# Kernel tuning notes

Hardware: AMD Instinct MI355X
Metric: run time of the kernel (lower is better)

## Reference

```python
import jax, jax.numpy as jnp
import numpy as np


def setup_inputs() -> dict:
    key = jax.random.key(0)
    k1, k2 = jax.random.split(key)
    in_features, out_features = 4096, 4096
    tokens = 8192
    x = jax.random.normal(k1, (tokens, in_features), dtype=jnp.float32)
    # matches reset_parameters: N(0, sqrt(1/in_features))
    weight = jax.random.normal(k2, (out_features, in_features), dtype=jnp.float32) * np.sqrt(1.0 / in_features)
    bias = jnp.zeros((out_features,), dtype=jnp.float32)
    return {"x": x, "weight": weight, "bias": bias}


def reference(x, weight, bias):
    # BinaryLinearFunction.forward: binarize weight to sign(w), dense matmul, add bias
    w_bin = jnp.sign(weight)  # [out, in], values in {-1, 0, +1}
    return x @ w_bin.T + bias  # [tokens, out]
```

## Files before the change

### kernel.cpp

```cpp
#include <hip/hip_runtime.h>
#include <stdint.h>
#include <stddef.h>

typedef int i32x4 __attribute__((ext_vector_type(4)));

static constexpr int M = 8192, N = 4096, K = 4096;
static constexpr int BM = 128, BN = 128, BK = 128;


__global__ __launch_bounds__(256) void quant_rows(const float* __restrict__ x,
                                                  int8_t* __restrict__ xq,
                                                  float* __restrict__ scales) {
    const int row = blockIdx.x;
    const int tid = threadIdx.x;
    const float4* xr = (const float4*)(x + (size_t)row * K);

    float4 v[4];
    float m = 0.f;
#pragma unroll
    for (int k = 0; k < 4; ++k) {
        v[k] = xr[k * 256 + tid];
        m = fmaxf(m, fmaxf(fmaxf(fabsf(v[k].x), fabsf(v[k].y)),
                           fmaxf(fabsf(v[k].z), fabsf(v[k].w))));
    }
#pragma unroll
    for (int off = 32; off; off >>= 1) m = fmaxf(m, __shfl_down(m, off, 64));

    __shared__ float wm[4];
    if ((tid & 63) == 0) wm[tid >> 6] = m;
    __syncthreads();
    const float amax = fmaxf(fmaxf(fmaxf(wm[0], wm[1]), fmaxf(wm[2], wm[3])), 1e-20f);
    const float s = 127.0f / amax;
    if (tid == 0) scales[row] = amax * (1.0f / 127.0f);

    int8_t* xo = xq + (size_t)row * K;
#pragma unroll
    for (int k = 0; k < 4; ++k) {
        int8_t o[4] = {(int8_t)__float2int_rn(v[k].x * s),
                       (int8_t)__float2int_rn(v[k].y * s),
                       (int8_t)__float2int_rn(v[k].z * s),
                       (int8_t)__float2int_rn(v[k].w * s)};
        *(int*)(xo + (k * 256 + tid) * 4) = *(const int*)o;
    }
}

__global__ __launch_bounds__(256) void binarize_w_kernel(const float* __restrict__ w,
                                                         int8_t* __restrict__ wq) {
    const size_t i = (size_t)blockIdx.x * 256 + threadIdx.x;
    float4 a = ((const float4*)w)[i];
    float vv[4] = {a.x, a.y, a.z, a.w};
    int8_t o[4];
#pragma unroll
    for (int j = 0; j < 4; ++j)
        o[j] = (vv[j] > 0.f) ? (int8_t)1 : ((vv[j] < 0.f) ? (int8_t)-1 : (int8_t)0);
    *(int*)(wq + 4 * i) = *(const int*)o;
}


__device__ __forceinline__ void async_copy16(const int8_t* g, int8_t* l) {
    __builtin_amdgcn_global_load_lds(
        (const __attribute__((address_space(1))) void*)g,
        (__attribute__((address_space(3))) void*)l,
        16, 0, 0);
}

__global__ __launch_bounds__(256) void gemm_i8(const int8_t* __restrict__ A,
                                               const int8_t* __restrict__ B,
                                               const float* __restrict__ bias,
                                               const float* __restrict__ scales,
                                               float* __restrict__ C) {
    __shared__ __align__(16) int8_t As[BM * BK];
    __shared__ __align__(16) int8_t Bs[BN * BK];

    const int tid  = threadIdx.x;
    const int lane = tid & 63;
    const int wave = tid >> 6;
    const int m0 = blockIdx.y * BM;
    const int n0 = blockIdx.x * BN;

    const int wr = wave >> 1, wc = wave & 1;
    const int q  = lane >> 4;
    const int lr = lane & 15;

    i32x4 acc[4][4];
#pragma unroll
    for (int i = 0; i < 4; ++i)
#pragma unroll
        for (int j = 0; j < 4; ++j) acc[i][j] = (i32x4)0;

    const int8_t* gA[4];
    const int8_t* gB[4];
#pragma unroll
    for (int j = 0; j < 4; ++j) {
        int s = tid + 256 * j;
        int r = s >> 3, c = s & 7;
        int cs = c ^ (r & 7);
        gA[j] = A + (size_t)(m0 + r) * K + cs * 16;
        gB[j] = B + (size_t)(n0 + r) * K + cs * 16;
    }

    int aoff[4], boff[4];
#pragma unroll
    for (int mi = 0; mi < 4; ++mi) {
        int r  = wr * 64 + mi * 16 + lr;
        aoff[mi] = (r * 8 + (q ^ (r & 7))) * 16;
        int rb = wc * 64 + mi * 16 + lr;
        boff[mi] = (rb * 8 + (q ^ (rb & 7))) * 16;
    }

    for (int kt = 0; kt < K / BK; ++kt) {
        const int kofs = kt * BK;
#pragma unroll
        for (int j = 0; j < 4; ++j) async_copy16(gA[j] + kofs, As + (tid + 256 * j) * 16);
#pragma unroll
        for (int j = 0; j < 4; ++j) async_copy16(gB[j] + kofs, Bs + (tid + 256 * j) * 16);
        __syncthreads();

#pragma unroll
        for (int ks = 0; ks < 2; ++ks) {
            const int kx = ks << 6;
            i32x4 af[4], bfr[4];
#pragma unroll
            for (int mi = 0; mi < 4; ++mi) af[mi]  = *(const i32x4*)(As + (aoff[mi] ^ kx));
#pragma unroll
            for (int ni = 0; ni < 4; ++ni) bfr[ni] = *(const i32x4*)(Bs + (boff[ni] ^ kx));
#pragma unroll
            for (int mi = 0; mi < 4; ++mi)
#pragma unroll
                for (int ni = 0; ni < 4; ++ni)
                    acc[mi][ni] = __builtin_amdgcn_mfma_i32_16x16x64_i8(
                        af[mi], bfr[ni], acc[mi][ni], 0, 0, 0);
        }
        __syncthreads();
    }

    float srow[4][4];
#pragma unroll
    for (int mi = 0; mi < 4; ++mi) {
        int row0 = m0 + wr * 64 + mi * 16 + q * 4;
#pragma unroll
        for (int i = 0; i < 4; ++i) srow[mi][i] = scales[row0 + i];
    }
#pragma unroll
    for (int ni = 0; ni < 4; ++ni) {
        int col = n0 + wc * 64 + ni * 16 + lr;
        float bv = bias[col];
#pragma unroll
        for (int mi = 0; mi < 4; ++mi) {
            int row0 = m0 + wr * 64 + mi * 16 + q * 4;
#pragma unroll
            for (int i = 0; i < 4; ++i)
                C[(size_t)(row0 + i) * N + col] = (float)acc[mi][ni][i] * srow[mi][i] + bv;
        }
    }
}


extern "C" void kernel_launch(void* const* d_in, const int* in_sizes, int n_in,
                              void* d_out, int out_size, void* d_ws, size_t ws_size,
                              hipStream_t stream) {
    const float* x    = (const float*)d_in[0];
    const float* w    = (const float*)d_in[1];
    const float* bias = (const float*)d_in[2];
    float* out        = (float*)d_out;

    float* scales = (float*)d_ws;
    int8_t* xq = (int8_t*)d_ws + 32768;
    int8_t* wq = xq + (size_t)M * K;

    quant_rows<<<M, 256, 0, stream>>>(x, xq, scales);
    binarize_w_kernel<<<(N * K / 4) / 256, 256, 0, stream>>>(w, wq);

    dim3 grid(N / BN, M / BM);
    gemm_i8<<<grid, 256, 0, stream>>>(xq, wq, bias, scales, out);
}
```

Baseline: 414.1 us.

## Double-buffer 256x256 int8 GEMM tiles with async LDS prefetch and block swizzle

Enlarges the GEMM tile to 256x256 with 512 threads, splits each K step into two 64-wide halves held in double-buffered shared memory, and prefetches the next stages with async global-to-LDS copies paced by explicit vmcnt waits. It also swizzles the block order on a 1D grid for L2 reuse and raises wave priority around MFMA bursts. The aim is to overlap memory loads with MFMA work and cut redundant global traffic. In exchange it uses much more LDS per block, which limits occupancy, and depends on hand-written waitcnt correctness.

```diff
diff --git a/kernel.cpp b/kernel.cpp
--- a/kernel.cpp
+++ b/kernel.cpp
@@ -5,7 +5,8 @@
 typedef int i32x4 __attribute__((ext_vector_type(4)));
 
 static constexpr int M = 8192, N = 4096, K = 4096;
-static constexpr int BM = 128, BN = 128, BK = 128;
+static constexpr int BM = 256, BN = 256, BK = 128;
+static constexpr int NT = K / BK;
 
 
 __global__ __launch_bounds__(256) void quant_rows(const float* __restrict__ x,
@@ -64,90 +65,136 @@
         16, 0, 0);
 }
 
-__global__ __launch_bounds__(256) void gemm_i8(const int8_t* __restrict__ A,
-                                               const int8_t* __restrict__ B,
-                                               const float* __restrict__ bias,
-                                               const float* __restrict__ scales,
-                                               float* __restrict__ C) {
-    __shared__ __align__(16) int8_t As[BM * BK];
-    __shared__ __align__(16) int8_t Bs[BN * BK];
+#define FENCE() asm volatile("" ::: "memory")
+#define BAR() do { FENCE(); __builtin_amdgcn_s_barrier(); FENCE(); } while (0)
+#define WAITVM(NN) asm volatile("s_waitcnt vmcnt(" #NN ")" ::: "memory")
+
+__global__ __launch_bounds__(512, 2) void gemm_i8(const int8_t* __restrict__ A,
+                                                  const int8_t* __restrict__ B,
+                                                  const float* __restrict__ bias,
+                                                  const float* __restrict__ scales,
+                                                  float* __restrict__ C) {
+    __shared__ __align__(16) int8_t As[2][2][BM * 64];
+    __shared__ __align__(16) int8_t Bs[2][2][BN * 64];
 
     const int tid  = threadIdx.x;
     const int lane = tid & 63;
     const int wave = tid >> 6;
-    const int m0 = blockIdx.y * BM;
-    const int n0 = blockIdx.x * BN;
-
-    const int wr = wave >> 1, wc = wave & 1;
+    const int wr = wave >> 2;
+    const int wc = wave & 3;
     const int q  = lane >> 4;
     const int lr = lane & 15;
 
-    i32x4 acc[4][4];
-#pragma unroll
-    for (int i = 0; i < 4; ++i)
-#pragma unroll
-        for (int j = 0; j < 4; ++j) acc[i][j] = (i32x4)0;
-
-    const int8_t* gA[4];
-    const int8_t* gB[4];
-#pragma unroll
-    for (int j = 0; j < 4; ++j) {
-        int s = tid + 256 * j;
-        int r = s >> 3, c = s & 7;
-        int cs = c ^ (r & 7);
-        gA[j] = A + (size_t)(m0 + r) * K + cs * 16;
-        gB[j] = B + (size_t)(n0 + r) * K + cs * 16;
-    }
-
-    int aoff[4], boff[4];
-#pragma unroll
-    for (int mi = 0; mi < 4; ++mi) {
-        int r  = wr * 64 + mi * 16 + lr;
-        aoff[mi] = (r * 8 + (q ^ (r & 7))) * 16;
-        int rb = wc * 64 + mi * 16 + lr;
-        boff[mi] = (rb * 8 + (q ^ (rb & 7))) * 16;
-    }
-
-    for (int kt = 0; kt < K / BK; ++kt) {
-        const int kofs = kt * BK;
-#pragma unroll
-        for (int j = 0; j < 4; ++j) async_copy16(gA[j] + kofs, As + (tid + 256 * j) * 16);
-#pragma unroll
-        for (int j = 0; j < 4; ++j) async_copy16(gB[j] + kofs, Bs + (tid + 256 * j) * 16);
-        __syncthreads();
-
-#pragma unroll
-        for (int ks = 0; ks < 2; ++ks) {
-            const int kx = ks << 6;
-            i32x4 af[4], bfr[4];
-#pragma unroll
-            for (int mi = 0; mi < 4; ++mi) af[mi]  = *(const i32x4*)(As + (aoff[mi] ^ kx));
-#pragma unroll
-            for (int ni = 0; ni < 4; ++ni) bfr[ni] = *(const i32x4*)(Bs + (boff[ni] ^ kx));
-#pragma unroll
-            for (int mi = 0; mi < 4; ++mi)
+    const int wg  = blockIdx.x;
+    const int swz = (wg & 7) * 64 + (wg >> 3);
+    const int m0  = (swz >> 4) * BM;
+    const int n0  = (swz & 15) * BN;
+
+    i32x4 acc[8][4];
+#pragma unroll
+    for (int mi = 0; mi < 8; ++mi)
+#pragma unroll
+        for (int ni = 0; ni < 4; ++ni) acc[mi][ni] = (i32x4)0;
+
+    int aoff[8], boff[4];
+#pragma unroll
+    for (int mi = 0; mi < 8; ++mi) {
+        const int r = wr * 128 + mi * 16 + lr;
+        aoff[mi] = r * 64 + ((q ^ (r & 3)) * 16);
+    }
+#pragma unroll
+    for (int ni = 0; ni < 4; ++ni) {
+        const int r = wc * 64 + ni * 16 + lr;
+        boff[ni] = r * 64 + ((q ^ (r & 3)) * 16);
+    }
+
+    const int s0 = tid, s1 = tid + 512;
+    const int8_t* sA0 = A + (size_t)(m0 + (s0 >> 2)) * K + (((s0 & 3) ^ ((s0 >> 2) & 3)) * 16);
+    const int8_t* sA1 = A + (size_t)(m0 + (s1 >> 2)) * K + (((s1 & 3) ^ ((s1 >> 2) & 3)) * 16);
+    const int8_t* sB0 = B + (size_t)(n0 + (s0 >> 2)) * K + (((s0 & 3) ^ ((s0 >> 2) & 3)) * 16);
+    const int8_t* sB1 = B + (size_t)(n0 + (s1 >> 2)) * K + (((s1 & 3) ^ ((s1 >> 2) & 3)) * 16);
+
+#define STAGE(buf, kh, kt) do {                                    \
+        const int _ko = (kt) * BK + (kh) * 64;                     \
+        async_copy16(sA0 + _ko, &As[buf][kh][s0 * 16]);            \
+        async_copy16(sA1 + _ko, &As[buf][kh][s1 * 16]);            \
+        async_copy16(sB0 + _ko, &Bs[buf][kh][s0 * 16]);            \
+        async_copy16(sB1 + _ko, &Bs[buf][kh][s1 * 16]);            \
+    } while (0)
+
+    STAGE(0, 0, 0);
+    STAGE(0, 1, 0);
+    STAGE(1, 0, 1);
+    WAITVM(8);
+    BAR();
+
+#pragma unroll 2
+    for (int t = 0; t < NT; ++t) {
+        const int cur = t & 1;
+        const int nxt = cur ^ 1;
+
+        {
+            const int8_t* Au = &As[cur][0][0];
+            const int8_t* Bu = &Bs[cur][0][0];
+            i32x4 af[8], bf[4];
+#pragma unroll
+            for (int mi = 0; mi < 8; ++mi) af[mi] = *(const i32x4*)(Au + aoff[mi]);
+#pragma unroll
+            for (int ni = 0; ni < 4; ++ni) bf[ni] = *(const i32x4*)(Bu + boff[ni]);
+            if (t + 1 < NT) STAGE(nxt, 1, t + 1);
+            BAR();
+            __builtin_amdgcn_s_setprio(1);
+#pragma unroll
+            for (int mi = 0; mi < 8; ++mi)
 #pragma unroll
                 for (int ni = 0; ni < 4; ++ni)
                     acc[mi][ni] = __builtin_amdgcn_mfma_i32_16x16x64_i8(
-                        af[mi], bfr[ni], acc[mi][ni], 0, 0, 0);
+                        af[mi], bf[ni], acc[mi][ni], 0, 0, 0);
+            __builtin_amdgcn_s_setprio(0);
+            if (t < NT - 1) { WAITVM(8); } else { WAITVM(0); }
+            BAR();
         }
-        __syncthreads();
-    }
-
-    float srow[4][4];
-#pragma unroll
-    for (int mi = 0; mi < 4; ++mi) {
-        int row0 = m0 + wr * 64 + mi * 16 + q * 4;
+
+        {
+            const int8_t* Au = &As[cur][1][0];
+            const int8_t* Bu = &Bs[cur][1][0];
+            i32x4 af[8], bf[4];
+#pragma unroll
+            for (int mi = 0; mi < 8; ++mi) af[mi] = *(const i32x4*)(Au + aoff[mi]);
+#pragma unroll
+            for (int ni = 0; ni < 4; ++ni) bf[ni] = *(const i32x4*)(Bu + boff[ni]);
+            if (t + 2 < NT) STAGE(cur, 0, t + 2);
+            BAR();
+            __builtin_amdgcn_s_setprio(1);
+#pragma unroll
+            for (int mi = 0; mi < 8; ++mi)
+#pragma unroll
+                for (int ni = 0; ni < 4; ++ni)
+                    acc[mi][ni] = __builtin_amdgcn_mfma_i32_16x16x64_i8(
+                        af[mi], bf[ni], acc[mi][ni], 0, 0, 0);
+            __builtin_amdgcn_s_setprio(0);
+            if (t < NT - 2) { WAITVM(8); }
+            else if (t == NT - 2) { WAITVM(4); }
+            else { WAITVM(0); }
+            BAR();
+        }
+    }
+#undef STAGE
+
+    float srow[8][4];
+#pragma unroll
+    for (int mi = 0; mi < 8; ++mi) {
+        const int row0 = m0 + wr * 128 + mi * 16 + q * 4;
 #pragma unroll
         for (int i = 0; i < 4; ++i) srow[mi][i] = scales[row0 + i];
     }
 #pragma unroll
     for (int ni = 0; ni < 4; ++ni) {
-        int col = n0 + wc * 64 + ni * 16 + lr;
-        float bv = bias[col];
-#pragma unroll
-        for (int mi = 0; mi < 4; ++mi) {
-            int row0 = m0 + wr * 64 + mi * 16 + q * 4;
+        const int col = n0 + wc * 64 + ni * 16 + lr;
+        const float bv = bias[col];
+#pragma unroll
+        for (int mi = 0; mi < 8; ++mi) {
+            const int row0 = m0 + wr * 128 + mi * 16 + q * 4;
 #pragma unroll
             for (int i = 0; i < 4; ++i)
                 C[(size_t)(row0 + i) * N + col] = (float)acc[mi][ni][i] * srow[mi][i] + bv;
@@ -171,6 +218,5 @@
     quant_rows<<<M, 256, 0, stream>>>(x, xq, scales);
     binarize_w_kernel<<<(N * K / 4) / 256, 256, 0, stream>>>(w, wq);
 
-    dim3 grid(N / BN, M / BM);
-    gemm_i8<<<grid, 256, 0, stream>>>(xq, wq, bias, scales, out);
-}
+    gemm_i8<<<dim3(512), 512, 0, stream>>>(xq, wq, bias, scales, out);
+}
```

Result: no change. 421.7 us (+1.8%).
